# Kernel optimization log

Measured on AMD Instinct MI355X. Metric: run time of the kernel, lower is better.

## Reference

```python
import jax, jax.numpy as jnp
import numpy as np

# batched graph: B graphs, each with N_PER_G nodes, fixed in-degree DEG
N_NODES = 51200
N_PER_G = 100
B = 512
DEG = 16
E = N_NODES * DEG
D_IN = 100   # input node feature dim
H1 = 100     # gc1 out
D_G = 20     # gc2 out / graph embedding dim
D_K = 32
P2D = 200    # dim_self_feat
P3D = 100    # dim_3d_feat
D_OUT = 1
LN_EPS = 1e-5


def setup_inputs() -> dict:
    key = jax.random.key(0)
    ks = jax.random.split(key, 24)
    feat = jax.random.normal(ks[0], (N_NODES, D_IN), jnp.float32)
    # every node has exactly DEG in-edges; sources drawn within the same graph
    edge_dst = jnp.repeat(jnp.arange(N_NODES, dtype=jnp.int32), DEG)
    off = jax.random.randint(ks[1], (E,), 0, N_PER_G, jnp.int32)
    edge_src = (edge_dst // N_PER_G) * N_PER_G + off
    self_feat = jax.random.normal(ks[2], (B, P2D), jnp.float32)
    x3d = jax.random.normal(ks[3], (B, P3D), jnp.float32)

    def lin(k, o, i):
        return jax.random.normal(k, (o, i), jnp.float32) / np.sqrt(i).astype(np.float32)

    params = dict(
        W1=lin(ks[4], H1, D_IN), b1=jnp.zeros((H1,), jnp.float32),
        W2=lin(ks[5], D_G, H1), b2=jnp.zeros((D_G,), jnp.float32),
        Wq2=lin(ks[6], D_K, D_G), Wk2=lin(ks[7], D_K, P2D),
        Wv2=lin(ks[8], D_K, P2D), Wo2=lin(ks[9], D_G, D_K),
        g2=jnp.ones((D_G,), jnp.float32), be2=jnp.zeros((D_G,), jnp.float32),
        Wq3=lin(ks[10], D_K, D_G), Wk3=lin(ks[11], D_K, P3D),
        Wv3=lin(ks[12], D_K, P3D), Wo3=lin(ks[13], D_G, D_K),
        g3=jnp.ones((D_G,), jnp.float32), be3=jnp.zeros((D_G,), jnp.float32),
        Wf1=lin(ks[14], 10, D_G), bf1=jnp.zeros((10,), jnp.float32),
        Wf2=lin(ks[15], D_OUT, 10), bf2=jnp.zeros((D_OUT,), jnp.float32),
    )
    return dict(feat=feat, edge_src=edge_src, edge_dst=edge_dst,
                self_feat=self_feat, x3d=x3d, **params)


def _gcn(h, src, dst, W, b):
    # copy_u -> mailbox mean (every node has exactly DEG in-edges) -> Linear
    msg = h[src]                                              # [E, d] gather
    acc = jax.ops.segment_sum(msg, dst, num_segments=N_NODES) / DEG
    return acc @ W.T + b


def _cross_attn(hg, x, Wq, Wk, Wv, Wo, gamma, beta):
    # K,V are single tokens -> softmax over length-1 axis is identically 1
    # so Z = V @ Wo^T exactly (Q/Wq does not affect the output values).
    Z = (x @ Wv.T) @ Wo.T                                     # [B, d_g]
    y = hg + Z
    mu = jnp.mean(y, axis=-1, keepdims=True)
    var = jnp.mean((y - mu) ** 2, axis=-1, keepdims=True)
    hg_attn = (y - mu) / jnp.sqrt(var + LN_EPS) * gamma + beta
    A = jnp.ones((hg.shape[0], 1), y.dtype)                   # softmax of (B,1,1)
    return hg_attn, A


def reference(feat, edge_src, edge_dst, self_feat, x3d,
              W1, b1, W2, b2,
              Wq2, Wk2, Wv2, Wo2, g2, be2,
              Wq3, Wk3, Wv3, Wo3, g3, be3,
              Wf1, bf1, Wf2, bf2):
    h = jax.nn.relu(_gcn(feat, edge_src, edge_dst, W1, b1))   # [N, 100]
    h = jax.nn.relu(_gcn(h, edge_src, edge_dst, W2, b2))      # [N, 20]
    hg = h.reshape(B, N_PER_G, D_G).mean(axis=1)              # dgl.mean_nodes
    hg1, _ = _cross_attn(hg, self_feat, Wq2, Wk2, Wv2, Wo2, g2, be2)
    hg2, _ = _cross_attn(hg1, x3d, Wq3, Wk3, Wv3, Wo3, g3, be3)
    out = jax.nn.relu(hg2 @ Wf1.T + bf1)
    out = out @ Wf2.T + bf2                                   # [B, 1]
    return out
```

## Files before the change

### kernel.cpp

```cpp
#include <hip/hip_runtime.h>
#include <hip/hip_bf16.h>

#define LN_EPS 1e-5f

typedef __attribute__((ext_vector_type(8))) short bf16x8;
typedef __attribute__((ext_vector_type(4))) float f32x4;

#define S 136
#define OFF_F  0
#define OFF_A  13600
#define OFF_S  28832
#define OFF_T2 33184
#define FLT    37536
#define ARENA_U 39360

#define FB1  300
#define FB2  400
#define FG2  420
#define FBE2 440
#define FG3  460
#define FBE3 480
#define FWF1 500
#define FBF1 700
#define FWF2 712
#define FBF2 724
#define FV2  728
#define FV3  760
#define FZ2  792
#define FZ3  812
#define FHGP 832

__device__ __forceinline__ unsigned short bf16rne(float x) {
    union { float f; unsigned u; } v; v.f = x;
    unsigned r = (v.u + 0x7FFFu + ((v.u >> 16) & 1u)) >> 16;
    return (unsigned short)r;
}

__device__ __forceinline__ unsigned pk2(float a, float b) {
    __hip_bfloat162 h = __float22bfloat162_rn(float2{a, b});
    unsigned r; __builtin_memcpy(&r, &h, 4); return r;
}

__device__ __forceinline__ void st4bf(unsigned short* p, const f32x4 v) {
    *(uint2*)p = make_uint2(pk2(v[0], v[1]), pk2(v[2], v[3]));
}

__device__ __forceinline__ bf16x8 pk8(const float4 a, const float4 b) {
    union { bf16x8 v; uint4 u; } r;
    r.u = make_uint4(pk2(a.x, a.y), pk2(a.z, a.w), pk2(b.x, b.y), pk2(b.z, b.w));
    return r.v;
}

template<int NT>
__device__ __forceinline__ void gemm_row(const unsigned short* __restrict__ ar,
    int Abase, int Bbase, int mrow, int lm, int lq, f32x4 (&acc)[NT])
{
    #pragma unroll
    for (int ks = 0; ks < 4; ++ks) {
        const int k = ks * 32 + lq * 8;
        bf16x8 a = *(const bf16x8*)&ar[Abase + (mrow * 16 + lm) * S + k];
        #pragma unroll
        for (int n = 0; n < NT; ++n) {
            bf16x8 b = *(const bf16x8*)&ar[Bbase + (n * 16 + lm) * S + k];
            acc[n] = __builtin_amdgcn_mfma_f32_16x16x32_bf16(a, b, acc[n], 0, 0, 0);
        }
    }
}

__global__ __launch_bounds__(512, 4) void fused_net_v7(
    const float* __restrict__ feat, const int* __restrict__ edge_src,
    const float* __restrict__ self_feat, const float* __restrict__ x3d,
    const float* __restrict__ W1, const float* __restrict__ b1,
    const float* __restrict__ W2, const float* __restrict__ b2,
    const float* __restrict__ Wv2, const float* __restrict__ Wo2,
    const float* __restrict__ g2, const float* __restrict__ be2,
    const float* __restrict__ Wv3, const float* __restrict__ Wo3,
    const float* __restrict__ g3, const float* __restrict__ be3,
    const float* __restrict__ Wf1, const float* __restrict__ bf1,
    const float* __restrict__ Wf2, const float* __restrict__ bf2,
    float* __restrict__ out)
{
    __shared__ __align__(16) unsigned short ar[ARENA_U];
    float* fl = (float*)&ar[FLT];

    const int g    = blockIdx.x;
    const int tid  = threadIdx.x;
    const int w    = tid >> 6;
    const int lane = tid & 63;
    const int lm   = lane & 15;
    const int lq   = lane >> 4;

    if (tid < 25)       *(float4*)&fl[FB1 + tid * 4]          = *(const float4*)&b1[tid * 4];
    else if (tid < 30)  *(float4*)&fl[FB2 + (tid - 25) * 4]   = *(const float4*)&b2[(tid - 25) * 4];
    else if (tid < 35)  *(float4*)&fl[FG2 + (tid - 30) * 4]   = *(const float4*)&g2[(tid - 30) * 4];
    else if (tid < 40)  *(float4*)&fl[FBE2 + (tid - 35) * 4]  = *(const float4*)&be2[(tid - 35) * 4];
    else if (tid < 45)  *(float4*)&fl[FG3 + (tid - 40) * 4]   = *(const float4*)&g3[(tid - 40) * 4];
    else if (tid < 50)  *(float4*)&fl[FBE3 + (tid - 45) * 4]  = *(const float4*)&be3[(tid - 45) * 4];
    else if (tid < 100) *(float4*)&fl[FWF1 + (tid - 50) * 4]  = *(const float4*)&Wf1[(tid - 50) * 4];
    else if (tid < 110) { const int j = tid - 100; fl[FBF1 + j] = bf1[j]; fl[FWF2 + j] = Wf2[j]; }
    else if (tid == 110) fl[FBF2] = bf2[0];

    if (w < 7) {
        bf16x8 afrag[4];
        {
            int am = w * 16 + lm; if (am > 99) am = 99;
            const float* frow = feat + g * 10000 + am * 100;
            #pragma unroll
            for (int ks = 0; ks < 3; ++ks) {
                const int k = ks * 32 + lq * 8;
                afrag[ks] = pk8(*(const float4*)&frow[k], *(const float4*)&frow[k + 4]);
            }
            const float4 z4 = make_float4(0.f, 0.f, 0.f, 0.f);
            afrag[3] = (lq == 0) ? pk8(*(const float4*)&frow[96], z4) : pk8(z4, z4);
        }

        for (int i = tid; i < 500; i += 448) {
            const int n = i / 25, k4 = (i % 25) * 4;
            const float4 v = *(const float4*)&W2[n * 100 + k4];
            *(uint2*)&ar[OFF_S + n * S + k4] = make_uint2(pk2(v.x, v.y), pk2(v.z, v.w));
        }
        for (int i = tid; i < 140; i += 448) {
            const int n = i / 7, j = (i % 7) * 4;
            *(uint2*)&ar[OFF_S + n * S + 100 + j] = make_uint2(0u, 0u);
        }
        for (int i = tid; i < 700; i += 448) {
            const int n = i / 7, j = (i % 7) * 4;
            *(uint2*)&ar[OFF_F + n * S + 100 + j] = make_uint2(0u, 0u);
        }
        for (int i = tid; i < 140; i += 448) {
            const int n = i / 7, j = (i % 7) * 4;
            *(uint2*)&ar[OFF_T2 + n * S + 100 + j] = make_uint2(0u, 0u);
        }

        f32x4 acc[7];
        {
            const f32x4 z = {0.f, 0.f, 0.f, 0.f};
            #pragma unroll
            for (int n = 0; n < 7; ++n) acc[n] = z;
        }
        #pragma unroll
        for (int ks = 0; ks < 3; ++ks) {
            const int k = ks * 32 + lq * 8;
            bf16x8 bf[7];
            #pragma unroll
            for (int n = 0; n < 7; ++n) {
                int brow = n * 16 + lm; if (brow > 99) brow = 99;
                const float* p = W1 + brow * 100 + k;
                bf[n] = pk8(*(const float4*)p, *(const float4*)(p + 4));
            }
            #pragma unroll
            for (int n = 0; n < 7; ++n)
                acc[n] = __builtin_amdgcn_mfma_f32_16x16x32_bf16(afrag[ks], bf[n], acc[n], 0, 0, 0);
        }
        {
            const float4 z4 = make_float4(0.f, 0.f, 0.f, 0.f);
            bf16x8 bf[7];
            #pragma unroll
            for (int n = 0; n < 7; ++n) {
                int brow = n * 16 + lm; if (brow > 99) brow = 99;
                const float4 a = (lq == 0) ? *(const float4*)&W1[brow * 100 + 96] : z4;
                bf[n] = pk8(a, z4);
            }
            #pragma unroll
            for (int n = 0; n < 7; ++n)
                acc[n] = __builtin_amdgcn_mfma_f32_16x16x32_bf16(afrag[3], bf[n], acc[n], 0, 0, 0);
        }
        {
            const int m0 = w * 16 + lq * 4;
            #pragma unroll
            for (int n = 0; n < 7; ++n) {
                const int cc = n * 16 + lm;
                if (cc < 100 && m0 <= 96) st4bf(&ar[OFF_F + cc * S + m0], acc[n]);
            }
        }
    } else {
        const int base = g * 100;
        int e1[16], e2[16];
        {
            const int* ep = edge_src + g * 1600 + lane * 16;
            int4 e;
            e = *(const int4*)&ep[0];  e1[0]=e.x;  e1[1]=e.y;  e1[2]=e.z;  e1[3]=e.w;
            e = *(const int4*)&ep[4];  e1[4]=e.x;  e1[5]=e.y;  e1[6]=e.z;  e1[7]=e.w;
            e = *(const int4*)&ep[8];  e1[8]=e.x;  e1[9]=e.y;  e1[10]=e.z; e1[11]=e.w;
            e = *(const int4*)&ep[12]; e1[12]=e.x; e1[13]=e.y; e1[14]=e.z; e1[15]=e.w;
            #pragma unroll
            for (int i = 0; i < 16; ++i) e1[i] -= base;
        }
        const bool r2 = (lane < 36);
        if (r2) {
            const int* ep = edge_src + g * 1600 + (64 + lane) * 16;
            int4 e;
            e = *(const int4*)&ep[0];  e2[0]=e.x;  e2[1]=e.y;  e2[2]=e.z;  e2[3]=e.w;
            e = *(const int4*)&ep[4];  e2[4]=e.x;  e2[5]=e.y;  e2[6]=e.z;  e2[7]=e.w;
            e = *(const int4*)&ep[8];  e2[8]=e.x;  e2[9]=e.y;  e2[10]=e.z; e2[11]=e.w;
            e = *(const int4*)&ep[12]; e2[12]=e.x; e2[13]=e.y; e2[14]=e.z; e2[15]=e.w;
            #pragma unroll
            for (int i = 0; i < 16; ++i) e2[i] -= base;
        }
        const int j = lane >> 1, h = lane & 1;
        {
            const float* wr = Wv2 + j * 200 + h * 100;
            const float* xr = self_feat + g * 200 + h * 100;
            float s = 0.f;
            for (int c = 0; c < 25; ++c) {
                const float4 a = *(const float4*)&wr[c * 4];
                const float4 x = *(const float4*)&xr[c * 4];
                s += a.x * x.x + a.y * x.y + a.z * x.z + a.w * x.w;
            }
            s += __shfl_xor(s, 1);
            if (h == 0) fl[FV2 + j] = s;
        }
        {
            const float* wr = Wv3 + j * 100;
            const float* xr = x3d + g * 100;
            const int c0 = h ? 13 : 0, c1 = h ? 25 : 13;
            float s = 0.f;
            for (int c = c0; c < c1; ++c) {
                const float4 a = *(const float4*)&wr[c * 4];
                const float4 x = *(const float4*)&xr[c * 4];
                s += a.x * x.x + a.y * x.y + a.z * x.z + a.w * x.w;
            }
            s += __shfl_xor(s, 1);
            if (h == 0) fl[FV3 + j] = s;
        }
        {
            const uint4 z4i = make_uint4(0u, 0u, 0u, 0u);
            const int r = lane;
            const int st = (r >> 3) % 17;
            #pragma unroll
            for (int pp = 0; pp < 17; ++pp) {
                int p = pp + st; if (p >= 17) p -= 17;
                *(uint4*)&ar[OFF_A + r * S + p * 8] = z4i;
            }
            #pragma unroll
            for (int i = 0; i < 16; ++i) {
                int cnt = 0;
                #pragma unroll
                for (int jj = 0; jj < 16; ++jj) cnt += (e1[jj] == e1[i]);
                ar[OFF_A + r * S + e1[i]] = bf16rne((float)cnt * 0.0625f);
            }
        }
        if (r2) {
            const uint4 z4i = make_uint4(0u, 0u, 0u, 0u);
            const int r = 64 + lane;
            const int st = (r >> 3) % 17;
            #pragma unroll
            for (int pp = 0; pp < 17; ++pp) {
                int p = pp + st; if (p >= 17) p -= 17;
                *(uint4*)&ar[OFF_A + r * S + p * 8] = z4i;
            }
            #pragma unroll
            for (int i = 0; i < 16; ++i) {
                int cnt = 0;
                #pragma unroll
                for (int jj = 0; jj < 16; ++jj) cnt += (e2[jj] == e2[i]);
                ar[OFF_A + r * S + e2[i]] = bf16rne((float)cnt * 0.0625f);
            }
        }
        if (lane < 20) {
            const float* wr = Wo2 + lane * 32;
            float s = 0.f;
            #pragma unroll
            for (int c = 0; c < 8; ++c) {
                const float4 a = *(const float4*)&wr[c * 4];
                s += a.x * fl[FV2 + c * 4] + a.y * fl[FV2 + c * 4 + 1]
                   + a.z * fl[FV2 + c * 4 + 2] + a.w * fl[FV2 + c * 4 + 3];
            }
            fl[FZ2 + lane] = s;
        } else if (lane < 40) {
            const int jz = lane - 20;
            const float* wr = Wo3 + jz * 32;
            float s = 0.f;
            #pragma unroll
            for (int c = 0; c < 8; ++c) {
                const float4 a = *(const float4*)&wr[c * 4];
                s += a.x * fl[FV3 + c * 4] + a.y * fl[FV3 + c * 4 + 1]
                   + a.z * fl[FV3 + c * 4 + 2] + a.w * fl[FV3 + c * 4 + 3];
            }
            fl[FZ3 + jz] = s;
        }
    }
    __syncthreads();

    f32x4 acc2[7];
    {
        const f32x4 z = {0.f, 0.f, 0.f, 0.f};
        #pragma unroll
        for (int n = 0; n < 7; ++n) acc2[n] = z;
    }
    if (w < 7) gemm_row<7>(ar, OFF_F, OFF_A, w, lm, lq, acc2);
    __syncthreads();

    if (w < 7) {
        const int m0 = w * 16 + lq * 4;
        if (m0 <= 96) {
            const float4 bb = *(const float4*)&fl[FB1 + m0];
            #pragma unroll
            for (int n = 0; n < 7; ++n) {
                const int cc = n * 16 + lm;
                if (cc < 100) {
                    f32x4 v = acc2[n];
                    v[0] = fmaxf(v[0] + bb.x, 0.f); v[1] = fmaxf(v[1] + bb.y, 0.f);
                    v[2] = fmaxf(v[2] + bb.z, 0.f); v[3] = fmaxf(v[3] + bb.w, 0.f);
                    st4bf(&ar[OFF_F + cc * S + m0], v);
                }
            }
        }
    }
    __syncthreads();

    const int mt  = w & 1;
    const int ntA = w >> 1;
    const bool hasB = (w < 6);
    const int ntB = 4 + (w >> 1);
    {
        const f32x4 z = {0.f, 0.f, 0.f, 0.f};
        f32x4 cA = z, cB = z;
        #pragma unroll
        for (int ks = 0; ks < 4; ++ks) {
            const int k = ks * 32 + lq * 8;
            bf16x8 a = *(const bf16x8*)&ar[OFF_S + (mt * 16 + lm) * S + k];
            bf16x8 bA = *(const bf16x8*)&ar[OFF_F + (ntA * 16 + lm) * S + k];
            cA = __builtin_amdgcn_mfma_f32_16x16x32_bf16(a, bA, cA, 0, 0, 0);
            if (hasB) {
                bf16x8 bB = *(const bf16x8*)&ar[OFF_F + (ntB * 16 + lm) * S + k];
                cB = __builtin_amdgcn_mfma_f32_16x16x32_bf16(a, bB, cB, 0, 0, 0);
            }
        }
        const int ccA = ntA * 16 + lm;
        if (ccA < 100) {
            #pragma unroll
            for (int r = 0; r < 4; ++r) {
                const int f2 = mt * 16 + lq * 4 + r;
                if (f2 < 20) ar[OFF_T2 + f2 * S + ccA] = bf16rne(cA[r]);
            }
        }
        if (hasB) {
            const int ccB = ntB * 16 + lm;
            if (ccB < 100) {
                #pragma unroll
                for (int r = 0; r < 4; ++r) {
                    const int f2 = mt * 16 + lq * 4 + r;
                    if (f2 < 20) ar[OFF_T2 + f2 * S + ccB] = bf16rne(cB[r]);
                }
            }
        }
    }
    __syncthreads();

    {
        const f32x4 z = {0.f, 0.f, 0.f, 0.f};
        f32x4 cA = z, cB = z;
        #pragma unroll
        for (int ks = 0; ks < 4; ++ks) {
            const int k = ks * 32 + lq * 8;
            bf16x8 a = *(const bf16x8*)&ar[OFF_T2 + (mt * 16 + lm) * S + k];
            bf16x8 bA = *(const bf16x8*)&ar[OFF_A + (ntA * 16 + lm) * S + k];
            cA = __builtin_amdgcn_mfma_f32_16x16x32_bf16(a, bA, cA, 0, 0, 0);
            if (hasB) {
                bf16x8 bB = *(const bf16x8*)&ar[OFF_A + (ntB * 16 + lm) * S + k];
                cB = __builtin_amdgcn_mfma_f32_16x16x32_bf16(a, bB, cB, 0, 0, 0);
            }
        }
        const int ccA = ntA * 16 + lm;
        const int ccB = ntB * 16 + lm;
        #pragma unroll
        for (int r = 0; r < 4; ++r) {
            const int f2 = mt * 16 + lq * 4 + r;
            const bool fv = (f2 < 20);
            const float bias = fv ? fl[FB2 + (fv ? f2 : 0)] : 0.f;
            float val = (fv && ccA < 100) ? fmaxf(cA[r] + bias, 0.f) : 0.f;
            if (hasB && fv && ccB < 100) val += fmaxf(cB[r] + bias, 0.f);
            val += __shfl_xor(val, 1);
            val += __shfl_xor(val, 2);
            val += __shfl_xor(val, 4);
            val += __shfl_xor(val, 8);
            if (lm == 0 && fv) fl[FHGP + (w >> 1) * 20 + f2] = val;
        }
    }
    __syncthreads();

    if (tid < 64) {
        const int j = tid;
        float y = 0.f;
        if (j < 20) {
            y = fl[FHGP + j] + fl[FHGP + 20 + j] + fl[FHGP + 40 + j] + fl[FHGP + 60 + j];
            y = y * 0.01f + fl[FZ2 + j];
        }
        float s = y;
        s += __shfl_xor(s, 1); s += __shfl_xor(s, 2); s += __shfl_xor(s, 4);
        s += __shfl_xor(s, 8); s += __shfl_xor(s, 16);
        const float mu = s * 0.05f;
        float d = (j < 20) ? (y - mu) : 0.f;
        float v = d * d;
        v += __shfl_xor(v, 1); v += __shfl_xor(v, 2); v += __shfl_xor(v, 4);
        v += __shfl_xor(v, 8); v += __shfl_xor(v, 16);
        const float inv1 = 1.f / sqrtf(v * 0.05f + LN_EPS);
        float y2 = 0.f;
        if (j < 20) y2 = d * inv1 * fl[FG2 + j] + fl[FBE2 + j] + fl[FZ3 + j];
        float s2 = y2;
        s2 += __shfl_xor(s2, 1); s2 += __shfl_xor(s2, 2); s2 += __shfl_xor(s2, 4);
        s2 += __shfl_xor(s2, 8); s2 += __shfl_xor(s2, 16);
        const float mu2 = s2 * 0.05f;
        float d2 = (j < 20) ? (y2 - mu2) : 0.f;
        float v2 = d2 * d2;
        v2 += __shfl_xor(v2, 1); v2 += __shfl_xor(v2, 2); v2 += __shfl_xor(v2, 4);
        v2 += __shfl_xor(v2, 8); v2 += __shfl_xor(v2, 16);
        const float inv2 = 1.f / sqrtf(v2 * 0.05f + LN_EPS);
        float y3 = 0.f;
        if (j < 20) y3 = d2 * inv2 * fl[FG3 + j] + fl[FBE3 + j];

        float acc7 = 0.f;
        {
            const int js = (j < 10) ? j : 0;
            #pragma unroll
            for (int k = 0; k < 20; ++k) {
                const float yk = __shfl(y3, k);
                acc7 += fl[FWF1 + js * 20 + k] * yk;
            }
            const float bias = fl[FBF1 + js];
            const float w2v  = fl[FWF2 + js];
            acc7 = (j < 10) ? fmaxf(acc7 + bias, 0.f) * w2v : 0.f;
        }
        acc7 += __shfl_xor(acc7, 1); acc7 += __shfl_xor(acc7, 2);
        acc7 += __shfl_xor(acc7, 4); acc7 += __shfl_xor(acc7, 8);
        if (j == 0) out[g] = acc7 + fl[FBF2];
    }
}

extern "C" void kernel_launch(void* const* d_in, const int* in_sizes, int n_in,
                              void* d_out, int out_size, void* d_ws, size_t ws_size,
                              hipStream_t stream) {
    const float* feat      = (const float*)d_in[0];
    const int*   edge_src  = (const int*)  d_in[1];
    const float* self_feat = (const float*)d_in[3];
    const float* x3d       = (const float*)d_in[4];
    const float* W1  = (const float*)d_in[5];
    const float* b1  = (const float*)d_in[6];
    const float* W2  = (const float*)d_in[7];
    const float* b2  = (const float*)d_in[8];
    const float* Wv2 = (const float*)d_in[11];
    const float* Wo2 = (const float*)d_in[12];
    const float* g2  = (const float*)d_in[13];
    const float* be2 = (const float*)d_in[14];
    const float* Wv3 = (const float*)d_in[17];
    const float* Wo3 = (const float*)d_in[18];
    const float* g3  = (const float*)d_in[19];
    const float* be3 = (const float*)d_in[20];
    const float* Wf1 = (const float*)d_in[21];
    const float* bf1 = (const float*)d_in[22];
    const float* Wf2 = (const float*)d_in[23];
    const float* bf2 = (const float*)d_in[24];

    fused_net_v7<<<512, 512, 0, stream>>>(feat, edge_src, self_feat, x3d,
                                          W1, b1, W2, b2,
                                          Wv2, Wo2, g2, be2,
                                          Wv3, Wo3, g3, be3,
                                          Wf1, bf1, Wf2, bf2,
                                          (float*)d_out);
}
```

Baseline: 136.9 us.

## Double block to 1024 threads and split GEMM N-tiles across wave pairs

Moves from 512 to 1024 threads per block. Each matrix-row wave is now split into two waves that each handle about half of the N tiles, and one extra wave is dedicated to edge-index loading and building the adjacency matrix. W1 is staged once into shared memory as bf16, replacing the per-wave global reads and conversions. Per-wave serial MFMA chains shrink and the shared-memory footprint drops. The cost is an extra block barrier and heavier scheduling per block, and the 1024-thread, 8-blocks launch bound could limit registers per thread.

```diff
diff --git a/kernel.cpp b/kernel.cpp
--- a/kernel.cpp
+++ b/kernel.cpp
@@ -9,26 +9,26 @@
 #define S 136
 #define OFF_F  0
 #define OFF_A  13600
-#define OFF_S  28832
-#define OFF_T2 33184
-#define FLT    37536
-#define ARENA_U 39360
-
-#define FB1  300
-#define FB2  400
-#define FG2  420
-#define FBE2 440
-#define FG3  460
-#define FBE3 480
-#define FWF1 500
-#define FBF1 700
-#define FWF2 712
-#define FBF2 724
-#define FV2  728
-#define FV3  760
-#define FZ2  792
-#define FZ3  812
-#define FHGP 832
+#define OFF_S  27200
+#define OFF_T2 29920
+#define FLT    32640
+#define ARENA_U 34304
+
+#define FB1  0
+#define FB2  100
+#define FG2  120
+#define FBE2 140
+#define FG3  160
+#define FBE3 180
+#define FWF1 200
+#define FBF1 400
+#define FWF2 412
+#define FBF2 424
+#define FV2  428
+#define FV3  460
+#define FZ2  492
+#define FZ3  512
+#define FHGP 532
 
 __device__ __forceinline__ unsigned short bf16rne(float x) {
     union { float f; unsigned u; } v; v.f = x;
@@ -51,23 +51,7 @@
     return r.v;
 }
 
-template<int NT>
-__device__ __forceinline__ void gemm_row(const unsigned short* __restrict__ ar,
-    int Abase, int Bbase, int mrow, int lm, int lq, f32x4 (&acc)[NT])
-{
-    #pragma unroll
-    for (int ks = 0; ks < 4; ++ks) {
-        const int k = ks * 32 + lq * 8;
-        bf16x8 a = *(const bf16x8*)&ar[Abase + (mrow * 16 + lm) * S + k];
-        #pragma unroll
-        for (int n = 0; n < NT; ++n) {
-            bf16x8 b = *(const bf16x8*)&ar[Bbase + (n * 16 + lm) * S + k];
-            acc[n] = __builtin_amdgcn_mfma_f32_16x16x32_bf16(a, b, acc[n], 0, 0, 0);
-        }
-    }
-}
-
-__global__ __launch_bounds__(512, 4) void fused_net_v7(
+__global__ __launch_bounds__(1024, 8) void fused_net_v8(
     const float* __restrict__ feat, const int* __restrict__ edge_src,
     const float* __restrict__ self_feat, const float* __restrict__ x3d,
     const float* __restrict__ W1, const float* __restrict__ b1,
@@ -90,6 +74,16 @@
     const int lm   = lane & 15;
     const int lq   = lane >> 4;
 
+    const int mw  = w >> 1;
+    const int nh  = w & 1;
+    const int nlo = nh ? 4 : 0;
+    const int nnt = nh ? 3 : 4;
+    const int mt  = w & 1;
+    const int nt3 = w >> 1;
+
+    bf16x8 afrag[4];
+    int e1[16], e2[16];
+
     if (tid < 25)       *(float4*)&fl[FB1 + tid * 4]          = *(const float4*)&b1[tid * 4];
     else if (tid < 30)  *(float4*)&fl[FB2 + (tid - 25) * 4]   = *(const float4*)&b2[(tid - 25) * 4];
     else if (tid < 35)  *(float4*)&fl[FG2 + (tid - 30) * 4]   = *(const float4*)&g2[(tid - 30) * 4];
@@ -100,103 +94,92 @@
     else if (tid < 110) { const int j = tid - 100; fl[FBF1 + j] = bf1[j]; fl[FWF2 + j] = Wf2[j]; }
     else if (tid == 110) fl[FBF2] = bf2[0];
 
-    if (w < 7) {
-        bf16x8 afrag[4];
-        {
-            int am = w * 16 + lm; if (am > 99) am = 99;
-            const float* frow = feat + g * 10000 + am * 100;
-            #pragma unroll
-            for (int ks = 0; ks < 3; ++ks) {
-                const int k = ks * 32 + lq * 8;
-                afrag[ks] = pk8(*(const float4*)&frow[k], *(const float4*)&frow[k + 4]);
-            }
-            const float4 z4 = make_float4(0.f, 0.f, 0.f, 0.f);
-            afrag[3] = (lq == 0) ? pk8(*(const float4*)&frow[96], z4) : pk8(z4, z4);
-        }
-
-        for (int i = tid; i < 500; i += 448) {
-            const int n = i / 25, k4 = (i % 25) * 4;
-            const float4 v = *(const float4*)&W2[n * 100 + k4];
-            *(uint2*)&ar[OFF_S + n * S + k4] = make_uint2(pk2(v.x, v.y), pk2(v.z, v.w));
-        }
-        for (int i = tid; i < 140; i += 448) {
-            const int n = i / 7, j = (i % 7) * 4;
-            *(uint2*)&ar[OFF_S + n * S + 100 + j] = make_uint2(0u, 0u);
-        }
-        for (int i = tid; i < 700; i += 448) {
-            const int n = i / 7, j = (i % 7) * 4;
-            *(uint2*)&ar[OFF_F + n * S + 100 + j] = make_uint2(0u, 0u);
-        }
-        for (int i = tid; i < 140; i += 448) {
-            const int n = i / 7, j = (i % 7) * 4;
-            *(uint2*)&ar[OFF_T2 + n * S + 100 + j] = make_uint2(0u, 0u);
-        }
-
-        f32x4 acc[7];
+    if (w < 14) {
+        int am = mw * 16 + lm; if (am > 99) am = 99;
+        const float* frow = feat + g * 10000 + am * 100;
+        #pragma unroll
+        for (int ks = 0; ks < 3; ++ks) {
+            const int k = ks * 32 + lq * 8;
+            afrag[ks] = pk8(*(const float4*)&frow[k], *(const float4*)&frow[k + 4]);
+        }
+        const float4 z4 = make_float4(0.f, 0.f, 0.f, 0.f);
+        afrag[3] = (lq == 0) ? pk8(*(const float4*)&frow[96], z4) : pk8(z4, z4);
+    } else if (w == 14) {
+        const int base = g * 100;
+        const int* ep = edge_src + g * 1600 + lane * 16;
+        int4 e;
+        e = *(const int4*)&ep[0];  e1[0]=e.x;  e1[1]=e.y;  e1[2]=e.z;  e1[3]=e.w;
+        e = *(const int4*)&ep[4];  e1[4]=e.x;  e1[5]=e.y;  e1[6]=e.z;  e1[7]=e.w;
+        e = *(const int4*)&ep[8];  e1[8]=e.x;  e1[9]=e.y;  e1[10]=e.z; e1[11]=e.w;
+        e = *(const int4*)&ep[12]; e1[12]=e.x; e1[13]=e.y; e1[14]=e.z; e1[15]=e.w;
+        #pragma unroll
+        for (int i = 0; i < 16; ++i) e1[i] -= base;
+        if (lane < 36) {
+            const int* ep2 = edge_src + g * 1600 + (64 + lane) * 16;
+            e = *(const int4*)&ep2[0];  e2[0]=e.x;  e2[1]=e.y;  e2[2]=e.z;  e2[3]=e.w;
+            e = *(const int4*)&ep2[4];  e2[4]=e.x;  e2[5]=e.y;  e2[6]=e.z;  e2[7]=e.w;
+            e = *(const int4*)&ep2[8];  e2[8]=e.x;  e2[9]=e.y;  e2[10]=e.z; e2[11]=e.w;
+            e = *(const int4*)&ep2[12]; e2[12]=e.x; e2[13]=e.y; e2[14]=e.z; e2[15]=e.w;
+            #pragma unroll
+            for (int i = 0; i < 16; ++i) e2[i] -= base;
+        }
+    }
+
+    for (int i = tid; i < 2500; i += 1024) {
+        const int n = i / 25, k4 = (i % 25) * 4;
+        const float4 v = *(const float4*)&W1[n * 100 + k4];
+        *(uint2*)&ar[OFF_A + n * S + k4] = make_uint2(pk2(v.x, v.y), pk2(v.z, v.w));
+    }
+    for (int i = tid; i < 700; i += 1024) {
+        const int n = i / 7, j = (i % 7) * 4;
+        *(uint2*)&ar[OFF_A + n * S + 100 + j] = make_uint2(0u, 0u);
+    }
+    for (int i = tid; i < 700; i += 1024) {
+        const int n = i / 7, j = (i % 7) * 4;
+        *(uint2*)&ar[OFF_F + n * S + 100 + j] = make_uint2(0u, 0u);
+    }
+    for (int i = tid; i < 500; i += 1024) {
+        const int n = i / 25, k4 = (i % 25) * 4;
+        const float4 v = *(const float4*)&W2[n * 100 + k4];
+        *(uint2*)&ar[OFF_S + n * S + k4] = make_uint2(pk2(v.x, v.y), pk2(v.z, v.w));
+    }
+    for (int i = tid; i < 140; i += 1024) {
+        const int n = i / 7, j = (i % 7) * 4;
+        *(uint2*)&ar[OFF_S + n * S + 100 + j] = make_uint2(0u, 0u);
+    }
+    for (int i = tid; i < 140; i += 1024) {
+        const int n = i / 7, j = (i % 7) * 4;
+        *(uint2*)&ar[OFF_T2 + n * S + 100 + j] = make_uint2(0u, 0u);
+    }
+    __syncthreads();
+
+    if (w < 14) {
+        f32x4 acc[4];
         {
             const f32x4 z = {0.f, 0.f, 0.f, 0.f};
             #pragma unroll
-            for (int n = 0; n < 7; ++n) acc[n] = z;
-        }
-        #pragma unroll
-        for (int ks = 0; ks < 3; ++ks) {
+            for (int n = 0; n < 4; ++n) acc[n] = z;
+        }
+        #pragma unroll
+        for (int ks = 0; ks < 4; ++ks) {
             const int k = ks * 32 + lq * 8;
-            bf16x8 bf[7];
-            #pragma unroll
-            for (int n = 0; n < 7; ++n) {
-                int brow = n * 16 + lm; if (brow > 99) brow = 99;
-                const float* p = W1 + brow * 100 + k;
-                bf[n] = pk8(*(const float4*)p, *(const float4*)(p + 4));
-            }
-            #pragma unroll
-            for (int n = 0; n < 7; ++n)
-                acc[n] = __builtin_amdgcn_mfma_f32_16x16x32_bf16(afrag[ks], bf[n], acc[n], 0, 0, 0);
-        }
-        {
-            const float4 z4 = make_float4(0.f, 0.f, 0.f, 0.f);
-            bf16x8 bf[7];
-            #pragma unroll
-            for (int n = 0; n < 7; ++n) {
-                int brow = n * 16 + lm; if (brow > 99) brow = 99;
-                const float4 a = (lq == 0) ? *(const float4*)&W1[brow * 100 + 96] : z4;
-                bf[n] = pk8(a, z4);
-            }
-            #pragma unroll
-            for (int n = 0; n < 7; ++n)
-                acc[n] = __builtin_amdgcn_mfma_f32_16x16x32_bf16(afrag[3], bf[n], acc[n], 0, 0, 0);
-        }
-        {
-            const int m0 = w * 16 + lq * 4;
-            #pragma unroll
-            for (int n = 0; n < 7; ++n) {
-                const int cc = n * 16 + lm;
+            #pragma unroll
+            for (int n = 0; n < 4; ++n) {
+                if (n < nnt) {
+                    bf16x8 b = *(const bf16x8*)&ar[OFF_A + ((nlo + n) * 16 + lm) * S + k];
+                    acc[n] = __builtin_amdgcn_mfma_f32_16x16x32_bf16(afrag[ks], b, acc[n], 0, 0, 0);
+                }
+            }
+        }
+        const int m0 = mw * 16 + lq * 4;
+        #pragma unroll
+        for (int n = 0; n < 4; ++n) {
+            if (n < nnt) {
+                const int cc = (nlo + n) * 16 + lm;
                 if (cc < 100 && m0 <= 96) st4bf(&ar[OFF_F + cc * S + m0], acc[n]);
             }
         }
-    } else {
-        const int base = g * 100;
-        int e1[16], e2[16];
-        {
-            const int* ep = edge_src + g * 1600 + lane * 16;
-            int4 e;
-            e = *(const int4*)&ep[0];  e1[0]=e.x;  e1[1]=e.y;  e1[2]=e.z;  e1[3]=e.w;
-            e = *(const int4*)&ep[4];  e1[4]=e.x;  e1[5]=e.y;  e1[6]=e.z;  e1[7]=e.w;
-            e = *(const int4*)&ep[8];  e1[8]=e.x;  e1[9]=e.y;  e1[10]=e.z; e1[11]=e.w;
-            e = *(const int4*)&ep[12]; e1[12]=e.x; e1[13]=e.y; e1[14]=e.z; e1[15]=e.w;
-            #pragma unroll
-            for (int i = 0; i < 16; ++i) e1[i] -= base;
-        }
-        const bool r2 = (lane < 36);
-        if (r2) {
-            const int* ep = edge_src + g * 1600 + (64 + lane) * 16;
-            int4 e;
-            e = *(const int4*)&ep[0];  e2[0]=e.x;  e2[1]=e.y;  e2[2]=e.z;  e2[3]=e.w;
-            e = *(const int4*)&ep[4];  e2[4]=e.x;  e2[5]=e.y;  e2[6]=e.z;  e2[7]=e.w;
-            e = *(const int4*)&ep[8];  e2[8]=e.x;  e2[9]=e.y;  e2[10]=e.z; e2[11]=e.w;
-            e = *(const int4*)&ep[12]; e2[12]=e.x; e2[13]=e.y; e2[14]=e.z; e2[15]=e.w;
-            #pragma unroll
-            for (int i = 0; i < 16; ++i) e2[i] -= base;
-        }
+    } else if (w == 15) {
         const int j = lane >> 1, h = lane & 1;
         {
             const float* wr = Wv2 + j * 200 + h * 100;
@@ -223,8 +206,12 @@
             s += __shfl_xor(s, 1);
             if (h == 0) fl[FV3 + j] = s;
         }
+    }
+    __syncthreads();
+
+    if (w == 14) {
+        const uint4 z4i = make_uint4(0u, 0u, 0u, 0u);
         {
-            const uint4 z4i = make_uint4(0u, 0u, 0u, 0u);
             const int r = lane;
             const int st = (r >> 3) % 17;
             #pragma unroll
@@ -240,8 +227,7 @@
                 ar[OFF_A + r * S + e1[i]] = bf16rne((float)cnt * 0.0625f);
             }
         }
-        if (r2) {
-            const uint4 z4i = make_uint4(0u, 0u, 0u, 0u);
+        if (lane < 36) {
             const int r = 64 + lane;
             const int st = (r >> 3) % 17;
             #pragma unroll
@@ -257,6 +243,7 @@
                 ar[OFF_A + r * S + e2[i]] = bf16rne((float)cnt * 0.0625f);
             }
         }
+    } else if (w == 15) {
         if (lane < 20) {
             const float* wr = Wo2 + lane * 32;
             float s = 0.f;
@@ -282,100 +269,91 @@
     }
     __syncthreads();
 
-    f32x4 acc2[7];
+    f32x4 acc2[4];
     {
         const f32x4 z = {0.f, 0.f, 0.f, 0.f};
         #pragma unroll
-        for (int n = 0; n < 7; ++n) acc2[n] = z;
-    }
-    if (w < 7) gemm_row<7>(ar, OFF_F, OFF_A, w, lm, lq, acc2);
-    __syncthreads();
-
-    if (w < 7) {
-        const int m0 = w * 16 + lq * 4;
+        for (int n = 0; n < 4; ++n) acc2[n] = z;
+    }
+    if (w < 14) {
+        #pragma unroll
+        for (int ks = 0; ks < 4; ++ks) {
+            const int k = ks * 32 + lq * 8;
+            bf16x8 a = *(const bf16x8*)&ar[OFF_F + (mw * 16 + lm) * S + k];
+            #pragma unroll
+            for (int n = 0; n < 4; ++n) {
+                if (n < nnt) {
+                    bf16x8 b = *(const bf16x8*)&ar[OFF_A + ((nlo + n) * 16 + lm) * S + k];
+                    acc2[n] = __builtin_amdgcn_mfma_f32_16x16x32_bf16(a, b, acc2[n], 0, 0, 0);
+                }
+            }
+        }
+    }
+    __syncthreads();
+
+    if (w < 14) {
+        const int m0 = mw * 16 + lq * 4;
         if (m0 <= 96) {
             const float4 bb = *(const float4*)&fl[FB1 + m0];
             #pragma unroll
-            for (int n = 0; n < 7; ++n) {
-                const int cc = n * 16 + lm;
-                if (cc < 100) {
-                    f32x4 v = acc2[n];
-                    v[0] = fmaxf(v[0] + bb.x, 0.f); v[1] = fmaxf(v[1] + bb.y, 0.f);
-                    v[2] = fmaxf(v[2] + bb.z, 0.f); v[3] = fmaxf(v[3] + bb.w, 0.f);
-                    st4bf(&ar[OFF_F + cc * S + m0], v);
+            for (int n = 0; n < 4; ++n) {
+                if (n < nnt) {
+                    const int cc = (nlo + n) * 16 + lm;
+                    if (cc < 100) {
+                        f32x4 v = acc2[n];
+                        v[0] = fmaxf(v[0] + bb.x, 0.f); v[1] = fmaxf(v[1] + bb.y, 0.f);
+                        v[2] = fmaxf(v[2] + bb.z, 0.f); v[3] = fmaxf(v[3] + bb.w, 0.f);
+                        st4bf(&ar[OFF_F + cc * S + m0], v);
+                    }
                 }
             }
         }
     }
     __syncthreads();
 
-    const int mt  = w & 1;
-    const int ntA = w >> 1;
-    const bool hasB = (w < 6);
-    const int ntB = 4 + (w >> 1);
-    {
+    if (w < 14) {
         const f32x4 z = {0.f, 0.f, 0.f, 0.f};
-        f32x4 cA = z, cB = z;
+        f32x4 c = z;
         #pragma unroll
         for (int ks = 0; ks < 4; ++ks) {
             const int k = ks * 32 + lq * 8;
             bf16x8 a = *(const bf16x8*)&ar[OFF_S + (mt * 16 + lm) * S + k];
-            bf16x8 bA = *(const bf16x8*)&ar[OFF_F + (ntA * 16 + lm) * S + k];
-            cA = __builtin_amdgcn_mfma_f32_16x16x32_bf16(a, bA, cA, 0, 0, 0);
-            if (hasB) {
-                bf16x8 bB = *(const bf16x8*)&ar[OFF_F + (ntB * 16 + lm) * S + k];
-                cB = __builtin_amdgcn_mfma_f32_16x16x32_bf16(a, bB, cB, 0, 0, 0);
-            }
-        }
-        const int ccA = ntA * 16 + lm;
-        if (ccA < 100) {
+            bf16x8 b = *(const bf16x8*)&ar[OFF_F + (nt3 * 16 + lm) * S + k];
+            c = __builtin_amdgcn_mfma_f32_16x16x32_bf16(a, b, c, 0, 0, 0);
+        }
+        const int cc = nt3 * 16 + lm;
+        if (cc < 100) {
             #pragma unroll
             for (int r = 0; r < 4; ++r) {
                 const int f2 = mt * 16 + lq * 4 + r;
-                if (f2 < 20) ar[OFF_T2 + f2 * S + ccA] = bf16rne(cA[r]);
-            }
-        }
-        if (hasB) {
-            const int ccB = ntB * 16 + lm;
-            if (ccB < 100) {
-                #pragma unroll
-                for (int r = 0; r < 4; ++r) {
-                    const int f2 = mt * 16 + lq * 4 + r;
-                    if (f2 < 20) ar[OFF_T2 + f2 * S + ccB] = bf16rne(cB[r]);
-                }
-            }
-        }
-    }
-    __syncthreads();
-
-    {
+                if (f2 < 20) ar[OFF_T2 + f2 * S + cc] = bf16rne(c[r]);
+            }
+        }
+    }
+    __syncthreads();
+
+    if (w < 14) {
         const f32x4 z = {0.f, 0.f, 0.f, 0.f};
-        f32x4 cA = z, cB = z;
+        f32x4 c = z;
         #pragma unroll
         for (int ks = 0; ks < 4; ++ks) {
             const int k = ks * 32 + lq * 8;
             bf16x8 a = *(const bf16x8*)&ar[OFF_T2 + (mt * 16 + lm) * S + k];
-            bf16x8 bA = *(const bf16x8*)&ar[OFF_A + (ntA * 16 + lm) * S + k];
-            cA = __builtin_amdgcn_mfma_f32_16x16x32_bf16(a, bA, cA, 0, 0, 0);
-            if (hasB) {
-                bf16x8 bB = *(const bf16x8*)&ar[OFF_A + (ntB * 16 + lm) * S + k];
-                cB = __builtin_amdgcn_mfma_f32_16x16x32_bf16(a, bB, cB, 0, 0, 0);
-            }
-        }
-        const int ccA = ntA * 16 + lm;
-        const int ccB = ntB * 16 + lm;
+            bf16x8 b = *(const bf16x8*)&ar[OFF_A + (nt3 * 16 + lm) * S + k];
+            c = __builtin_amdgcn_mfma_f32_16x16x32_bf16(a, b, c, 0, 0, 0);
+        }
+        const int cc = nt3 * 16 + lm;
         #pragma unroll
         for (int r = 0; r < 4; ++r) {
             const int f2 = mt * 16 + lq * 4 + r;
             const bool fv = (f2 < 20);
             const float bias = fv ? fl[FB2 + (fv ? f2 : 0)] : 0.f;
-            float val = (fv && ccA < 100) ? fmaxf(cA[r] + bias, 0.f) : 0.f;
-            if (hasB && fv && ccB < 100) val += fmaxf(cB[r] + bias, 0.f);
+            float val = (fv && cc < 100) ? fmaxf(c[r] + bias, 0.f) : 0.f;
             val += __shfl_xor(val, 1);
             val += __shfl_xor(val, 2);
             val += __shfl_xor(val, 4);
             val += __shfl_xor(val, 8);
-            if (lm == 0 && fv) fl[FHGP + (w >> 1) * 20 + f2] = val;
+            if (lm == 0 && fv) fl[FHGP + nt3 * 20 + f2] = val;
         }
     }
     __syncthreads();
@@ -384,7 +362,9 @@
         const int j = tid;
         float y = 0.f;
         if (j < 20) {
-            y = fl[FHGP + j] + fl[FHGP + 20 + j] + fl[FHGP + 40 + j] + fl[FHGP + 60 + j];
+            y = fl[FHGP + j];
+            #pragma unroll
+            for (int sft = 1; sft < 7; ++sft) y += fl[FHGP + sft * 20 + j];
             y = y * 0.01f + fl[FZ2 + j];
         }
         float s = y;
@@ -452,10 +432,10 @@
     const float* Wf2 = (const float*)d_in[23];
     const float* bf2 = (const float*)d_in[24];
 
-    fused_net_v7<<<512, 512, 0, stream>>>(feat, edge_src, self_feat, x3d,
-                                          W1, b1, W2, b2,
-                                          Wv2, Wo2, g2, be2,
-                                          Wv3, Wo3, g3, be3,
-                                          Wf1, bf1, Wf2, bf2,
-                                          (float*)d_out);
-}
+    fused_net_v8<<<512, 1024, 0, stream>>>(feat, edge_src, self_feat, x3d,
+                                           W1, b1, W2, b2,
+                                           Wv2, Wo2, g2, be2,
+                                           Wv3, Wo3, g3, be3,
+                                           Wf1, bf1, Wf2, bf2,
+                                           (float*)d_out);
+}
```

After: 133.7 us. -2.3%, faster.
